# Performance work log

Measured on AMD Instinct MI355X. Metric: run time of the kernel, lower is better.

## Reference

```python
import jax, jax.numpy as jnp
import numpy as np
import math

THETA = 1.0


def _qdense(xa, xb, wa, wb, ba, bb):
    # QComplexDense: j_squared = -cos(2*theta)
    j2 = -math.cos(2.0 * THETA)
    out_a = xa @ wa.T + j2 * (xb @ wb.T) + ba
    out_b = xa @ wb.T + xb @ wa.T + bb
    return out_a, out_b


def setup_inputs() -> dict:
    key = jax.random.key(0)
    B, S, D = 4, 2048, 1024
    ks = jax.random.split(key, 16)
    limit = math.sqrt(6.0 / (D + D))  # xavier uniform for square [D,D]

    def w(k):
        return jax.random.uniform(k, (D, D), jnp.float32, -limit, limit)

    inp = {
        'xa': jax.random.normal(ks[0], (B, S, D), jnp.float32),
        'xb': jax.random.normal(ks[1], (B, S, D), jnp.float32),
    }
    i = 2
    for n in ('q', 'k', 'v', 'o'):
        inp[n + '_wa'] = w(ks[i]); inp[n + '_wb'] = w(ks[i + 1])
        inp[n + '_ba'] = jnp.zeros((D,), jnp.float32)
        inp[n + '_bb'] = jnp.zeros((D,), jnp.float32)
        i += 2
    return inp


def reference(xa, xb,
              q_wa, q_wb, q_ba, q_bb,
              k_wa, k_wb, k_ba, k_bb,
              v_wa, v_wb, v_ba, v_bb,
              o_wa, o_wb, o_ba, o_bb):
    D = xa.shape[-1]
    # NOTE: qc_matmul in the original uses cos(2 * ones(1)) == cos(2.0),
    # a constant independent of theta.
    c2 = math.cos(2.0)

    Qa, Qb = _qdense(xa, xb, q_wa, q_wb, q_ba, q_bb)
    Ka, Kb = _qdense(xa, xb, k_wa, k_wb, k_ba, k_bb)
    Va, Vb = _qdense(xa, xb, v_wa, v_wb, v_ba, v_bb)

    # complex-style QK^T: scores_a = Qa Ka^T - cos(2) Qb Kb^T ; scores_b = Qa Kb^T + Qb Ka^T
    sa = jnp.einsum('bsd,btd->bst', Qa, Ka) - c2 * jnp.einsum('bsd,btd->bst', Qb, Kb)
    sb = jnp.einsum('bsd,btd->bst', Qa, Kb) + jnp.einsum('bsd,btd->bst', Qb, Ka)
    scores_real = jnp.sqrt(sa * sa + sb * sb)  # magnitude
    attn = jax.nn.softmax(scores_real / math.sqrt(D), axis=-1)  # [B,S,S]

    out_a = jnp.einsum('bst,btd->bsd', attn, Va)
    out_b = jnp.einsum('bst,btd->bsd', attn, Vb)
    return _qdense(out_a, out_b, o_wa, o_wb, o_ba, o_bb)
```

## Files before the change

### kernel.cpp

```cpp
#include <hip/hip_runtime.h>
#include <math.h>

typedef __bf16 bf16_t;
typedef __attribute__((ext_vector_type(4))) float f32x4;
typedef __attribute__((ext_vector_type(8))) __bf16 v8bf;
typedef __attribute__((ext_vector_type(4))) __bf16 v4bf;

#define GLOAD_LDS16(g, l)                                                     \
  __builtin_amdgcn_global_load_lds(                                           \
      (const __attribute__((address_space(1))) void*)(g),                     \
      (__attribute__((address_space(3))) void*)(l), 16, 0, 0)

__global__ void sentinel_kernel(float* o, float v) { o[0] = v; }

__global__ __launch_bounds__(256) void pack_x_kernel(
    const float* __restrict__ xa, const float* __restrict__ xb,
    bf16_t* __restrict__ xcat, int n4)
{
  int i = blockIdx.x * 256 + threadIdx.x;
  if (i >= n4) return;
  float4 a = reinterpret_cast<const float4*>(xa)[i];
  float4 b = reinterpret_cast<const float4*>(xb)[i];
  long e = (long)i * 4;
  long m = e >> 10;
  int  d = (int)(e & 1023);
  v4bf av = { (bf16_t)a.x, (bf16_t)a.y, (bf16_t)a.z, (bf16_t)a.w };
  v4bf bv = { (bf16_t)b.x, (bf16_t)b.y, (bf16_t)b.z, (bf16_t)b.w };
  *reinterpret_cast<v4bf*>(xcat + m * 2048 + d)        = av;
  *reinterpret_cast<v4bf*>(xcat + m * 2048 + 1024 + d) = bv;
}

__global__ __launch_bounds__(256) void pack_w_kernel(
    const float* __restrict__ wa, const float* __restrict__ wb,
    bf16_t* __restrict__ outA, bf16_t* __restrict__ outB, float j2)
{
  int i = blockIdx.x * 256 + threadIdx.x;
  float4 a = reinterpret_cast<const float4*>(wa)[i];
  float4 b = reinterpret_cast<const float4*>(wb)[i];
  long e = (long)i * 4;
  long n = e >> 10;
  int  k = (int)(e & 1023);
  v4bf av = { (bf16_t)a.x, (bf16_t)a.y, (bf16_t)a.z, (bf16_t)a.w };
  v4bf bv = { (bf16_t)b.x, (bf16_t)b.y, (bf16_t)b.z, (bf16_t)b.w };
  v4bf jb = { (bf16_t)(j2*b.x), (bf16_t)(j2*b.y), (bf16_t)(j2*b.z), (bf16_t)(j2*b.w) };
  *reinterpret_cast<v4bf*>(outA + n * 2048 + k)        = av;
  *reinterpret_cast<v4bf*>(outA + n * 2048 + 1024 + k) = jb;
  *reinterpret_cast<v4bf*>(outB + n * 2048 + k)        = bv;
  *reinterpret_cast<v4bf*>(outB + n * 2048 + 1024 + k) = av;
}

template<int EPI>
__global__ __launch_bounds__(512) void gemm256_kernel(
    const bf16_t* __restrict__ A, const bf16_t* __restrict__ B,
    int K, long lda, long ldb, long bsA, long bsB,
    void* __restrict__ o0p, void* __restrict__ o1p, void* __restrict__ o2p,
    const float* __restrict__ bb0, const float* __restrict__ bb1,
    const float* __restrict__ bb2, const float* __restrict__ bb3,
    const float* __restrict__ bb4, const float* __restrict__ bb5,
    float scl)
{
  __shared__ __align__(16) bf16_t lds[65536];
  const int tid  = threadIdx.x;
  const int wid  = tid >> 6;
  const int lane = tid & 63;
  const int rr = lane & 15;
  const int kg = lane >> 4;
  const int wm = wid >> 2;
  const int wn = wid & 3;
  const long row0 = (long)blockIdx.y * 256;
  const long col0 = (long)blockIdx.x * 256;
  const int z = blockIdx.z;
  const bf16_t* Ab = A + (long)z * bsA + row0 * lda;
  const bf16_t* Bb = B + (long)z * bsB + col0 * ldb;

  const int rhat = tid >> 2;
  const int scol = ((tid & 3) * 8) ^ (((rhat >> 1) & 3) << 3);
  const bf16_t* gA0 = Ab + (long)rhat * lda + scol;
  const bf16_t* gA1 = Ab + (long)(rhat + 128) * lda + scol;
  const bf16_t* gB0 = Bb + (long)rhat * ldb + scol;
  const bf16_t* gB1 = Bb + (long)(rhat + 128) * ldb + scol;
  const int dbase = wid * 512;

#define STAGE_A0(t_) GLOAD_LDS16(gA0 + (long)(t_) * 32, lds + ((t_) & 3) * 16384 +         dbase)
#define STAGE_A1(t_) GLOAD_LDS16(gA1 + (long)(t_) * 32, lds + ((t_) & 3) * 16384 +  4096 + dbase)
#define STAGE_B0(t_) GLOAD_LDS16(gB0 + (long)(t_) * 32, lds + ((t_) & 3) * 16384 +  8192 + dbase)
#define STAGE_B1(t_) GLOAD_LDS16(gB1 + (long)(t_) * 32, lds + ((t_) & 3) * 16384 + 12288 + dbase)

  const int kq = (kg * 8) ^ (((rr >> 1) & 3) << 3);
  const int abase = (wm * 128 + rr) * 32 + kq;
  const int bbase = 8192 + (wn * 64 + rr) * 32 + kq;

  f32x4 acc[8][4];
#pragma unroll
  for (int i = 0; i < 8; ++i)
#pragma unroll
    for (int j = 0; j < 4; ++j) acc[i][j] = (f32x4){0.f, 0.f, 0.f, 0.f};

  const int T = K >> 5;

  STAGE_A0(0); STAGE_A1(0); STAGE_B0(0); STAGE_B1(0);
  STAGE_A0(1); STAGE_A1(1); STAGE_B0(1); STAGE_B1(1);
  asm volatile("s_waitcnt vmcnt(4)" ::: "memory");
  __builtin_amdgcn_sched_barrier(0);
  __builtin_amdgcn_s_barrier();

  for (int t = 0; t < T; ++t) {
    const int slotE = (t & 3) * 16384;
    const bool pf = (t + 2) < T;
    v8bf ar[4], br[4];
#pragma unroll
    for (int j = 0; j < 4; ++j)
      br[j] = *reinterpret_cast<const v8bf*>(lds + slotE + bbase + j * 512);
#pragma unroll
    for (int i = 0; i < 4; ++i)
      ar[i] = *reinterpret_cast<const v8bf*>(lds + slotE + abase + i * 512);
    if (pf) { STAGE_A0(t + 2); STAGE_A1(t + 2); }
    __builtin_amdgcn_s_barrier();
    __builtin_amdgcn_s_setprio(1);
#pragma unroll
    for (int i = 0; i < 4; ++i)
#pragma unroll
      for (int j = 0; j < 4; ++j)
        acc[i][j] = __builtin_amdgcn_mfma_f32_16x16x32_bf16(ar[i], br[j], acc[i][j], 0, 0, 0);
    __builtin_amdgcn_s_setprio(0);
    __builtin_amdgcn_s_barrier();
#pragma unroll
    for (int i = 0; i < 4; ++i)
      ar[i] = *reinterpret_cast<const v8bf*>(lds + slotE + abase + (4 + i) * 512);
    if (pf) { STAGE_B0(t + 2); STAGE_B1(t + 2); }
    __builtin_amdgcn_s_barrier();
    __builtin_amdgcn_s_setprio(1);
#pragma unroll
    for (int i = 0; i < 4; ++i)
#pragma unroll
      for (int j = 0; j < 4; ++j)
        acc[4 + i][j] = __builtin_amdgcn_mfma_f32_16x16x32_bf16(ar[i], br[j], acc[4 + i][j], 0, 0, 0);
    __builtin_amdgcn_s_setprio(0);
    if (pf) { asm volatile("s_waitcnt vmcnt(4)" ::: "memory"); }
    else    { asm volatile("s_waitcnt vmcnt(0)" ::: "memory"); }
    __builtin_amdgcn_sched_barrier(0);
    __builtin_amdgcn_s_barrier();
  }
#undef STAGE_A0
#undef STAGE_A1
#undef STAGE_B0
#undef STAGE_B1

#pragma unroll
  for (int ii = 0; ii < 8; ++ii) {
    const long mrow = row0 + wm * 128 + ii * 16 + kg * 4;
#pragma unroll
    for (int j = 0; j < 4; ++j) {
      const long col = col0 + wn * 64 + j * 16 + rr;
#pragma unroll
      for (int r2 = 0; r2 < 4; ++r2) {
        const float v = acc[ii][j][r2];
        const long row = mrow + r2;
        if constexpr (EPI == 0) {
          const int  seg = (int)(col >> 10);
          const long c   = col & 1023;
          bf16_t* Q  = (bf16_t*)o0p;
          bf16_t* Kc = (bf16_t*)o1p;
          bf16_t* Vc = (bf16_t*)o2p;
          const long kbase = (row >> 11) * 8388608 + (row & 2047) * 2048;
          switch (seg) {
            case 0: Q[row * 2048 + c]        = (bf16_t)((v + bb0[c]) * 0.03125f); break;
            case 1: Q[row * 2048 + 1024 + c] = (bf16_t)((v + bb1[c]) * 0.03125f); break;
            case 2: { const float w = v + bb2[c];
                      Kc[kbase + c]                   = (bf16_t)w;
                      Kc[kbase + 4194304 + 1024 + c]  = (bf16_t)w;
                    } break;
            case 3: { const float w = v + bb3[c];
                      Kc[kbase + 4194304 + c]         = (bf16_t)w;
                      Kc[kbase + 1024 + c]            = (bf16_t)(scl * w);
                    } break;
            case 4: Vc[row * 2048 + c]        = (bf16_t)(v + bb4[c]); break;
            default: Vc[row * 2048 + 1024 + c] = (bf16_t)(v + bb5[c]); break;
          }
        } else if constexpr (EPI == 1) {
          const int  seg = (int)(col >> 11);
          const long c   = col & 2047;
          bf16_t* dst = seg ? (bf16_t*)o1p : (bf16_t*)o0p;
          dst[(long)z * 4194304 + row * 2048 + c] = (bf16_t)v;
        } else if constexpr (EPI == 2) {
          ((bf16_t*)o0p)[(long)z * 4194304 + row * 2048 + col] = (bf16_t)v;
        } else {
          const int  seg = (int)(col >> 10);
          const long c   = col & 1023;
          float* dst = seg ? (float*)o1p : (float*)o0p;
          const float bv = seg ? bb1[c] : bb0[c];
          dst[row * 1024 + c] = v + bv;
        }
      }
    }
  }
}

__global__ __launch_bounds__(256) void transpose_v_kernel(
    const bf16_t* __restrict__ src, bf16_t* __restrict__ dst,
    int srcoff, int dstoff)
{
  __shared__ bf16_t t[64][65];
  const int tid = threadIdx.x;
  const long c0 = (long)blockIdx.x * 64;
  const long g0 = (long)blockIdx.y * 64;
#pragma unroll
  for (int it = 0; it < 16; ++it) {
    int idx = it * 256 + tid;
    int r = idx >> 6, c = idx & 63;
    t[r][c] = src[(g0 + r) * 2048 + srcoff + c0 + c];
  }
  __syncthreads();
  const long b  = g0 >> 11;
  const long t0 = g0 & 2047;
#pragma unroll
  for (int it = 0; it < 16; ++it) {
    int idx = it * 256 + tid;
    int nr = idx >> 6, tc = idx & 63;
    dst[b * 4194304 + (dstoff + c0 + nr) * 2048 + t0 + tc] = t[tc][nr];
  }
}

__global__ __launch_bounds__(256) void softmax_mag_kernel(
    const bf16_t* __restrict__ sa, const bf16_t* __restrict__ sb,
    bf16_t* __restrict__ attn)
{
  const int tid = threadIdx.x;
  const long base = (long)blockIdx.x * 2048;
  v4bf a0 = *reinterpret_cast<const v4bf*>(sa + base + tid * 4);
  v4bf a1 = *reinterpret_cast<const v4bf*>(sa + base + 1024 + tid * 4);
  v4bf b0 = *reinterpret_cast<const v4bf*>(sb + base + tid * 4);
  v4bf b1 = *reinterpret_cast<const v4bf*>(sb + base + 1024 + tid * 4);
  float r[8];
#pragma unroll
  for (int k = 0; k < 4; ++k) {
    float x = (float)a0[k], y = (float)b0[k];
    r[k] = sqrtf(x * x + y * y);
  }
#pragma unroll
  for (int k = 0; k < 4; ++k) {
    float x = (float)a1[k], y = (float)b1[k];
    r[4 + k] = sqrtf(x * x + y * y);
  }
  float m = r[0];
#pragma unroll
  for (int k = 1; k < 8; ++k) m = fmaxf(m, r[k]);
#pragma unroll
  for (int off = 32; off > 0; off >>= 1) m = fmaxf(m, __shfl_xor(m, off));
  __shared__ float red[8];
  if ((tid & 63) == 0) red[tid >> 6] = m;
  __syncthreads();
  m = fmaxf(fmaxf(red[0], red[1]), fmaxf(red[2], red[3]));
  float p[8], s = 0.f;
#pragma unroll
  for (int k = 0; k < 8; ++k) { p[k] = __expf(r[k] - m); s += p[k]; }
#pragma unroll
  for (int off = 32; off > 0; off >>= 1) s += __shfl_xor(s, off);
  if ((tid & 63) == 0) red[4 + (tid >> 6)] = s;
  __syncthreads();
  const float inv = 1.f / (red[4] + red[5] + red[6] + red[7]);
  v4bf o0 = { (bf16_t)(p[0]*inv), (bf16_t)(p[1]*inv), (bf16_t)(p[2]*inv), (bf16_t)(p[3]*inv) };
  v4bf o1 = { (bf16_t)(p[4]*inv), (bf16_t)(p[5]*inv), (bf16_t)(p[6]*inv), (bf16_t)(p[7]*inv) };
  *reinterpret_cast<v4bf*>(attn + base + tid * 4)        = o0;
  *reinterpret_cast<v4bf*>(attn + base + 1024 + tid * 4) = o1;
}

extern "C" void kernel_launch(void* const* d_in, const int* in_sizes, int n_in,
                              void* d_out, int out_size, void* d_ws, size_t ws_size,
                              hipStream_t stream)
{
  (void)in_sizes; (void)n_in; (void)out_size;
  const float* xa = (const float*)d_in[0];
  const float* xb = (const float*)d_in[1];
  const float *w_a[4], *w_b[4], *b_a[4], *b_b[4];
  for (int p = 0; p < 4; ++p) {
    w_a[p] = (const float*)d_in[2 + p*4 + 0];
    w_b[p] = (const float*)d_in[2 + p*4 + 1];
    b_a[p] = (const float*)d_in[2 + p*4 + 2];
    b_b[p] = (const float*)d_in[2 + p*4 + 3];
  }
  float* out = (float*)d_out;
  const float neg_c2 = (float)(-cos(2.0));

  const size_t WFULL = 33554432ull;
  const size_t WQKV  = 25165824ull;
  int NB = 0; bool fullW = true;
  if      (ws_size >= WFULL + 6ull * 4ull * 8388608ull) NB = 4;
  else if (ws_size >= WFULL + 6ull * 2ull * 8388608ull) NB = 2;
  else if (ws_size >= WFULL + 6ull * 1ull * 8388608ull) NB = 1;
  else if (ws_size >= WQKV  + 6ull * 1ull * 8388608ull) { NB = 1; fullW = false; }
  else { sentinel_kernel<<<1, 1, 0, stream>>>(out, (float)ws_size); return; }

  char* ws = (char*)d_ws;
  const size_t wbytes = fullW ? WFULL : WQKV;
  const size_t RB = (size_t)NB * 8388608ull;
  bf16_t* Wqkv = (bf16_t*)ws;
  bf16_t* Wo   = fullW ? (bf16_t*)(ws + WQKV) : Wqkv;
  bf16_t* R0 = (bf16_t*)(ws + wbytes);
  bf16_t* R1 = (bf16_t*)(ws + wbytes + 1*RB);
  bf16_t* Kc = (bf16_t*)(ws + wbytes + 2*RB);
  bf16_t* R4 = (bf16_t*)(ws + wbytes + 4*RB);
  bf16_t* R5 = (bf16_t*)(ws + wbytes + 5*RB);

  const int  Mc = NB * 2048;
  const dim3 blk(256);
  const dim3 blk512(512);
  const dim3 gqkv(24, Mc / 256, 1);
  const dim3 gsc(16, 8, NB);
  const dim3 gpv(8, 8, NB);
  const dim3 go(8, Mc / 256, 1);
  const dim3 gtr(16, Mc / 64, 1);

  if (fullW) {
    for (int p = 0; p < 3; ++p)
      pack_w_kernel<<<1024, blk, 0, stream>>>(w_a[p], w_b[p],
          Wqkv + (size_t)(2*p)   * 2097152ull,
          Wqkv + (size_t)(2*p+1) * 2097152ull, neg_c2);
    pack_w_kernel<<<1024, blk, 0, stream>>>(w_a[3], w_b[3],
        Wo, Wo + 2097152ull, neg_c2);
  }

  for (int c = 0; c < 4 / NB; ++c) {
    const size_t xoff = (size_t)c * NB * 2097152ull;
    pack_x_kernel<<<Mc, blk, 0, stream>>>(xa + xoff, xb + xoff, R0, Mc * 256);

    if (!fullW)
      for (int p = 0; p < 3; ++p)
        pack_w_kernel<<<1024, blk, 0, stream>>>(w_a[p], w_b[p],
            Wqkv + (size_t)(2*p)   * 2097152ull,
            Wqkv + (size_t)(2*p+1) * 2097152ull, neg_c2);

    gemm256_kernel<0><<<gqkv, blk512, 0, stream>>>(R0, Wqkv, 2048, 2048, 2048, 0, 0,
        R1, Kc, R4, b_a[0], b_b[0], b_a[1], b_b[1], b_a[2], b_b[2], neg_c2);

    transpose_v_kernel<<<gtr, blk, 0, stream>>>(R4, R5, 0,    0);
    transpose_v_kernel<<<gtr, blk, 0, stream>>>(R4, R5, 1024, 1024);

    gemm256_kernel<1><<<gsc, blk512, 0, stream>>>(R1, Kc, 2048, 2048, 2048, 4194304, 8388608,
        R0, R4, nullptr, nullptr, nullptr, nullptr, nullptr, nullptr, nullptr, 0.f);

    softmax_mag_kernel<<<Mc, blk, 0, stream>>>(R0, R4, R0);

    gemm256_kernel<2><<<gpv, blk512, 0, stream>>>(R0, R5, 2048, 2048, 2048, 4194304, 4194304,
        R1, nullptr, nullptr, nullptr, nullptr, nullptr, nullptr, nullptr, nullptr, 0.f);

    if (!fullW)
      pack_w_kernel<<<1024, blk, 0, stream>>>(w_a[3], w_b[3], Wo, Wo + 2097152ull, neg_c2);
    gemm256_kernel<3><<<go, blk512, 0, stream>>>(R1, Wo, 2048, 2048, 2048, 0, 0,
        out + xoff, out + 8388608ull + xoff, nullptr,
        b_a[3], b_b[3], nullptr, nullptr, nullptr, nullptr, 0.f);
  }
}
```

Before: 606.4 us.

## Unroll GEMM main loop by four, drop intra-tile barriers, swizzle workgroup order

Rewrites the GEMM main loop as a four-way unrolled body with compile-time LDS slot offsets and incrementing global pointers, so per-iteration address arithmetic and the pf branch go away. It removes the two mid-tile s_barriers and loads the second A half into a separate register set, which lets the two MFMA halves overlap. It also remaps the workgroup index so that consecutive blocks are spread in groups of eight, aiming for better cache locality across XCDs. Dropping the barriers risks LDS races between the prefetch into slot t+2 and reads of the current slot, and the tail assumes T is a multiple of four and at least four.

```diff
diff --git a/kernel.cpp b/kernel.cpp
--- a/kernel.cpp
+++ b/kernel.cpp
@@ -6,10 +6,11 @@
 typedef __attribute__((ext_vector_type(8))) __bf16 v8bf;
 typedef __attribute__((ext_vector_type(4))) __bf16 v4bf;
 
-#define GLOAD_LDS16(g, l)                                                     \
+#define GLLDS(g, l)                                                           \
   __builtin_amdgcn_global_load_lds(                                           \
       (const __attribute__((address_space(1))) void*)(g),                     \
       (__attribute__((address_space(3))) void*)(l), 16, 0, 0)
+#define OPQ(p) asm volatile("" : "+v"(p))
 
 __global__ void sentinel_kernel(float* o, float v) { o[0] = v; }
 
@@ -67,8 +68,14 @@
   const int kg = lane >> 4;
   const int wm = wid >> 2;
   const int wn = wid & 3;
-  const long row0 = (long)blockIdx.y * 256;
-  const long col0 = (long)blockIdx.x * 256;
+
+  int flat = blockIdx.y * gridDim.x + blockIdx.x;
+  const int nwg = gridDim.x * gridDim.y;
+  flat = (flat & 7) * (nwg >> 3) + (flat >> 3);
+  const int bx = flat % gridDim.x;
+  const int by = flat / gridDim.x;
+  const long row0 = (long)by * 256;
+  const long col0 = (long)bx * 256;
   const int z = blockIdx.z;
   const bf16_t* Ab = A + (long)z * bsA + row0 * lda;
   const bf16_t* Bb = B + (long)z * bsB + col0 * ldb;
@@ -81,14 +88,11 @@
   const bf16_t* gB1 = Bb + (long)(rhat + 128) * ldb + scol;
   const int dbase = wid * 512;
 
-#define STAGE_A0(t_) GLOAD_LDS16(gA0 + (long)(t_) * 32, lds + ((t_) & 3) * 16384 +         dbase)
-#define STAGE_A1(t_) GLOAD_LDS16(gA1 + (long)(t_) * 32, lds + ((t_) & 3) * 16384 +  4096 + dbase)
-#define STAGE_B0(t_) GLOAD_LDS16(gB0 + (long)(t_) * 32, lds + ((t_) & 3) * 16384 +  8192 + dbase)
-#define STAGE_B1(t_) GLOAD_LDS16(gB1 + (long)(t_) * 32, lds + ((t_) & 3) * 16384 + 12288 + dbase)
-
   const int kq = (kg * 8) ^ (((rr >> 1) & 3) << 3);
-  const int abase = (wm * 128 + rr) * 32 + kq;
-  const int bbase = 8192 + (wn * 64 + rr) * 32 + kq;
+  const bf16_t* rdA  = lds + (wm * 128 + rr) * 32 + kq;
+  const bf16_t* rdB  = lds + 8192 + (wn * 64 + rr) * 32 + kq;
+  const bf16_t* rdA2 = rdA + 32768;
+  const bf16_t* rdB2 = rdB + 32768;
 
   f32x4 acc[8][4];
 #pragma unroll
@@ -98,53 +102,80 @@
 
   const int T = K >> 5;
 
-  STAGE_A0(0); STAGE_A1(0); STAGE_B0(0); STAGE_B1(0);
-  STAGE_A0(1); STAGE_A1(1); STAGE_B0(1); STAGE_B1(1);
+  const bf16_t* sA0 = gA0;
+  const bf16_t* sA1 = gA1;
+  const bf16_t* sB0 = gB0;
+  const bf16_t* sB1 = gB1;
+
+  GLLDS(sA0, lds + dbase);
+  GLLDS(sA1, lds + 4096 + dbase);
+  GLLDS(sB0, lds + 8192 + dbase);
+  GLLDS(sB1, lds + 12288 + dbase);
+  sA0 += 32; sA1 += 32; sB0 += 32; sB1 += 32;
+  OPQ(sA0); OPQ(sA1); OPQ(sB0); OPQ(sB1);
+  GLLDS(sA0, lds + 16384 + dbase);
+  GLLDS(sA1, lds + 16384 + 4096 + dbase);
+  GLLDS(sB0, lds + 16384 + 8192 + dbase);
+  GLLDS(sB1, lds + 16384 + 12288 + dbase);
+  sA0 += 32; sA1 += 32; sB0 += 32; sB1 += 32;
+  OPQ(sA0); OPQ(sA1); OPQ(sB0); OPQ(sB1);
   asm volatile("s_waitcnt vmcnt(4)" ::: "memory");
   __builtin_amdgcn_sched_barrier(0);
   __builtin_amdgcn_s_barrier();
 
-  for (int t = 0; t < T; ++t) {
-    const int slotE = (t & 3) * 16384;
-    const bool pf = (t + 2) < T;
-    v8bf ar[4], br[4];
-#pragma unroll
-    for (int j = 0; j < 4; ++j)
-      br[j] = *reinterpret_cast<const v8bf*>(lds + slotE + bbase + j * 512);
-#pragma unroll
-    for (int i = 0; i < 4; ++i)
-      ar[i] = *reinterpret_cast<const v8bf*>(lds + slotE + abase + i * 512);
-    if (pf) { STAGE_A0(t + 2); STAGE_A1(t + 2); }
-    __builtin_amdgcn_s_barrier();
-    __builtin_amdgcn_s_setprio(1);
-#pragma unroll
-    for (int i = 0; i < 4; ++i)
-#pragma unroll
-      for (int j = 0; j < 4; ++j)
-        acc[i][j] = __builtin_amdgcn_mfma_f32_16x16x32_bf16(ar[i], br[j], acc[i][j], 0, 0, 0);
-    __builtin_amdgcn_s_setprio(0);
-    __builtin_amdgcn_s_barrier();
-#pragma unroll
-    for (int i = 0; i < 4; ++i)
-      ar[i] = *reinterpret_cast<const v8bf*>(lds + slotE + abase + (4 + i) * 512);
-    if (pf) { STAGE_B0(t + 2); STAGE_B1(t + 2); }
-    __builtin_amdgcn_s_barrier();
-    __builtin_amdgcn_s_setprio(1);
-#pragma unroll
-    for (int i = 0; i < 4; ++i)
-#pragma unroll
-      for (int j = 0; j < 4; ++j)
-        acc[4 + i][j] = __builtin_amdgcn_mfma_f32_16x16x32_bf16(ar[i], br[j], acc[4 + i][j], 0, 0, 0);
-    __builtin_amdgcn_s_setprio(0);
-    if (pf) { asm volatile("s_waitcnt vmcnt(4)" ::: "memory"); }
-    else    { asm volatile("s_waitcnt vmcnt(0)" ::: "memory"); }
-    __builtin_amdgcn_sched_barrier(0);
-    __builtin_amdgcn_s_barrier();
-  }
-#undef STAGE_A0
-#undef STAGE_A1
-#undef STAGE_B0
-#undef STAGE_B1
+#define TILE_BODY(U, PF)                                                       \
+  {                                                                            \
+    const bf16_t* ra_ = ((U) < 2) ? rdA : rdA2;                                \
+    const bf16_t* rb_ = ((U) < 2) ? rdB : rdB2;                                \
+    v8bf ar[4], br[4], ar2[4];                                                 \
+    _Pragma("unroll")                                                          \
+    for (int j = 0; j < 4; ++j)                                                \
+      br[j] = *reinterpret_cast<const v8bf*>(rb_ + ((U) & 1) * 16384 + j * 512); \
+    _Pragma("unroll")                                                          \
+    for (int i = 0; i < 4; ++i)                                                \
+      ar[i] = *reinterpret_cast<const v8bf*>(ra_ + ((U) & 1) * 16384 + i * 512); \
+    if (PF) {                                                                  \
+      GLLDS(sA0, lds + (((U) + 2) & 3) * 16384 + dbase);                       \
+      GLLDS(sA1, lds + (((U) + 2) & 3) * 16384 + 4096 + dbase);                \
+    }                                                                          \
+    __builtin_amdgcn_s_setprio(1);                                             \
+    _Pragma("unroll")                                                          \
+    for (int i = 0; i < 4; ++i)                                                \
+      _Pragma("unroll")                                                        \
+      for (int j = 0; j < 4; ++j)                                              \
+        acc[i][j] = __builtin_amdgcn_mfma_f32_16x16x32_bf16(ar[i], br[j], acc[i][j], 0, 0, 0); \
+    _Pragma("unroll")                                                          \
+    for (int i = 0; i < 4; ++i)                                                \
+      ar2[i] = *reinterpret_cast<const v8bf*>(ra_ + ((U) & 1) * 16384 + (4 + i) * 512); \
+    if (PF) {                                                                  \
+      GLLDS(sB0, lds + (((U) + 2) & 3) * 16384 + 8192 + dbase);                \
+      GLLDS(sB1, lds + (((U) + 2) & 3) * 16384 + 12288 + dbase);               \
+      sA0 += 32; sA1 += 32; sB0 += 32; sB1 += 32;                              \
+      OPQ(sA0); OPQ(sA1); OPQ(sB0); OPQ(sB1);                                  \
+    }                                                                          \
+    _Pragma("unroll")                                                          \
+    for (int i = 0; i < 4; ++i)                                                \
+      _Pragma("unroll")                                                        \
+      for (int j = 0; j < 4; ++j)                                              \
+        acc[4 + i][j] = __builtin_amdgcn_mfma_f32_16x16x32_bf16(ar2[i], br[j], acc[4 + i][j], 0, 0, 0); \
+    __builtin_amdgcn_s_setprio(0);                                             \
+    if (PF) { asm volatile("s_waitcnt vmcnt(4)" ::: "memory"); }               \
+    else    { asm volatile("s_waitcnt vmcnt(0)" ::: "memory"); }               \
+    __builtin_amdgcn_sched_barrier(0);                                         \
+    __builtin_amdgcn_s_barrier();                                              \
+  }
+
+  for (int tb = 0; tb < T - 4; tb += 4) {
+    TILE_BODY(0, 1)
+    TILE_BODY(1, 1)
+    TILE_BODY(2, 1)
+    TILE_BODY(3, 1)
+  }
+  TILE_BODY(0, 1)
+  TILE_BODY(1, 1)
+  TILE_BODY(2, 0)
+  TILE_BODY(3, 0)
+#undef TILE_BODY
 
 #pragma unroll
   for (int ii = 0; ii < 8; ++ii) {
```

Result: faster. 564.9 us (-6.8%).
